# Kernel tuning notes

Hardware: AMD Instinct MI355X
Metric: run time of the kernel (lower is better)

The kernel has to match this reference:

```python
import jax, jax.numpy as jnp
import numpy as np

D_MODEL = 1024
N_HEADS = 16
D_K = D_MODEL // N_HEADS
THETA = 10000.0
B, S = 2, 2048


def _rope(x):
    # x: [B, H, S, Dh], interleaved-pair RoPE with positions arange(S)
    Dh = x.shape[-1]
    inv_freq = 1.0 / (THETA ** (jnp.arange(0, Dh, 2, dtype=jnp.float32) / Dh))  # [Dh/2]
    pos = jnp.arange(x.shape[-2], dtype=jnp.float32)
    ang = pos[:, None] * inv_freq[None, :]                      # [S, Dh/2]
    cos = jnp.repeat(jnp.cos(ang), 2, axis=-1).astype(x.dtype)  # [S, Dh]
    sin = jnp.repeat(jnp.sin(ang), 2, axis=-1).astype(x.dtype)
    # rotate pairs: (x_2k, x_2k+1) -> (-x_2k+1, x_2k)
    xp = x.reshape(*x.shape[:-1], Dh // 2, 2)
    rot = jnp.stack((-xp[..., 1], xp[..., 0]), axis=-1).reshape(x.shape)
    return x * cos + rot * sin


def setup_inputs() -> dict:
    key = jax.random.key(0)
    ks = jax.random.split(key, 5)
    std = (2.0 / (D_MODEL + D_MODEL)) ** 0.5
    return {
        "x": jax.random.normal(ks[0], (B, S, D_MODEL), dtype=jnp.float32),
        "wq": jax.random.normal(ks[1], (D_MODEL, D_MODEL), dtype=jnp.float32) * std,
        "wk": jax.random.normal(ks[2], (D_MODEL, D_MODEL), dtype=jnp.float32) * std,
        "wv": jax.random.normal(ks[3], (D_MODEL, D_MODEL), dtype=jnp.float32) * std,
        "wo": jax.random.normal(ks[4], (D_MODEL, D_MODEL), dtype=jnp.float32) * std,
    }


def reference(x, wq, wk, wv, wo):
    b, s, _ = x.shape
    def split_heads(t):
        return t.reshape(b, s, N_HEADS, D_K).transpose(0, 2, 1, 3)  # [B,H,S,Dk]
    # Linear: y = x @ W.T  (weights stored [out, in])
    q = split_heads(jnp.einsum('bsd,od->bso', x, wq))
    k = split_heads(jnp.einsum('bsd,od->bso', x, wk))
    v = split_heads(jnp.einsum('bsd,od->bso', x, wv))
    q = _rope(q)
    k = _rope(k)
    scores = jnp.einsum('bhqd,bhkd->bhqk', q, k) / jnp.sqrt(jnp.asarray(D_K, x.dtype))
    causal = jnp.tril(jnp.ones((s, s), dtype=bool))
    scores = jnp.where(causal[None, None], scores, -jnp.inf)
    attn = jax.nn.softmax(scores, axis=-1)
    out = jnp.einsum('bhqk,bhkd->bhqd', attn, v)
    out = out.transpose(0, 2, 1, 3).reshape(b, s, D_MODEL)
    return jnp.einsum('bsd,od->bso', out, wo)
```

## Files before the change

kernel.cpp:

```cpp
#include <hip/hip_runtime.h>


typedef unsigned short u16;
typedef __attribute__((ext_vector_type(8))) short short8;
typedef __attribute__((ext_vector_type(4))) float float4v;

typedef const __attribute__((address_space(1))) void GV;
typedef __attribute__((address_space(3))) void LV;

#define VSTR 72
#define QSCL 0.18033688011112042f

__device__ __forceinline__ u16 f2b(float f) {
    union { float f; unsigned int i; } t; t.f = f;
    unsigned int r = t.i + 0x7fffu + ((t.i >> 16) & 1u);
    return (u16)(r >> 16);
}

__global__ __launch_bounds__(256) void cvt_all(
    const float4* __restrict__ x,  const float4* __restrict__ wq,
    const float4* __restrict__ wk, const float4* __restrict__ wv,
    const float4* __restrict__ wo,
    u16* __restrict__ xb, u16* __restrict__ wcat, u16* __restrict__ wob)
{
    const int i = blockIdx.x * 256 + threadIdx.x;
    const float4* s; u16* d; int off;
    if (i < 524288) { s = x; d = xb; off = i; }
    else {
        const int widx = i - 524288;
        const int w = widx >> 17, o = widx & 131071;
        switch (w) {
            case 0:  s = wq; d = wcat;              break;
            case 1:  s = wk; d = wcat + (1 << 20);  break;
            case 2:  s = wv; d = wcat + (2 << 20);  break;
            default: s = wo; d = wob;               break;
        }
        off = o;
    }
    float4 a = s[2 * off], b = s[2 * off + 1];
    u16 t[8] = {f2b(a.x), f2b(a.y), f2b(a.z), f2b(a.w),
                f2b(b.x), f2b(b.y), f2b(b.z), f2b(b.w)};
    reinterpret_cast<int4*>(d)[off] = *reinterpret_cast<int4*>(t);
}

__global__ __launch_bounds__(256) void rope_tab(float2* __restrict__ tab) {
    const int i = blockIdx.x * 256 + threadIdx.x;
    const int pos = i >> 5, fi = i & 31;
    const float freq = exp2f((float)fi * -0.4152410118609203f);
    float sn, cs; sincosf((float)pos * freq, &sn, &cs);
    tab[i] = make_float2(cs, sn);
}

template<int NT, int ROPE, int NBLK>
__global__ __launch_bounds__(256) void gemm_tile(
    const u16* __restrict__ X, const u16* __restrict__ Wb,
    u16* __restrict__ Yq, u16* __restrict__ Yk, u16* __restrict__ Yv,
    float* __restrict__ Yf, const float2* __restrict__ tab)
{
    __shared__ u16 As[128 * 64];
    __shared__ u16 Bs[NT * 32 * 64];

    const int tid  = threadIdx.x;
    const int wave = tid >> 6;
    const int lane = tid & 63;
    const int quad = lane >> 4;
    const int l16  = lane & 15;
    const int wm = (wave >> 1) * 64, wn = (wave & 1) * (NT * 16);
    const int g = blockIdx.x;
    const int rr = g >> 3;
    const int m0 = ((g & 7) * 4 + rr / NBLK) * 128;
    const int n0 = (rr % NBLK) * (NT * 32);
    const int lrow = lane >> 3;
    const int cg8  = (lane & 7) ^ lrow;

    float4v acc[4][NT];
#pragma unroll
    for (int mt = 0; mt < 4; mt++)
#pragma unroll
        for (int nt = 0; nt < NT; nt++) acc[mt][nt] = (float4v){0.f, 0.f, 0.f, 0.f};

    for (int kb = 0; kb < 1024; kb += 64) {
        __syncthreads();
#pragma unroll
        for (int t = 0; t < 4; t++) {
            const int I = wave * 4 + t;
            const u16* gp = X + (size_t)(m0 + I * 8 + lrow) * 1024 + kb + cg8 * 8;
            __builtin_amdgcn_global_load_lds((GV*)gp, (LV*)&As[I * 512], 16, 0, 0);
        }
#pragma unroll
        for (int t = 0; t < NT; t++) {
            const int I = wave * NT + t;
            const u16* gp = Wb + (size_t)(n0 + I * 8 + lrow) * 1024 + kb + cg8 * 8;
            __builtin_amdgcn_global_load_lds((GV*)gp, (LV*)&Bs[I * 512], 16, 0, 0);
        }
        __syncthreads();
#pragma unroll
        for (int ks = 0; ks < 2; ks++) {
            const int su = ((ks * 4 + quad) ^ (l16 & 7)) * 8;
            short8 af[4], bf[NT];
#pragma unroll
            for (int t = 0; t < 4; t++)
                af[t] = *reinterpret_cast<const short8*>(&As[(wm + t * 16 + l16) * 64 + su]);
#pragma unroll
            for (int t = 0; t < NT; t++)
                bf[t] = *reinterpret_cast<const short8*>(&Bs[(wn + t * 16 + l16) * 64 + su]);
#pragma unroll
            for (int mt = 0; mt < 4; mt++)
#pragma unroll
                for (int nt = 0; nt < NT; nt++)
                    acc[mt][nt] = __builtin_amdgcn_mfma_f32_16x16x32_bf16(af[mt], bf[nt], acc[mt][nt], 0, 0, 0);
        }
    }

    if (ROPE) {
#pragma unroll
        for (int nt = 0; nt < NT; nt++) {
            const int cg = n0 + wn + nt * 16 + l16;
            const int buf = cg >> 10;
            const int c = cg & 1023;
            u16* dst = (buf == 0) ? Yq : ((buf == 1) ? Yk : Yv);
            const bool rp = (buf < 2);
            const float scl = (buf == 0) ? QSCL : 1.0f;
            const int fi = (cg & 63) >> 1;
#pragma unroll
            for (int mt = 0; mt < 4; mt++)
#pragma unroll
                for (int r = 0; r < 4; r++) {
                    const int row = m0 + wm + mt * 16 + quad * 4 + r;
                    float v = acc[mt][nt][r];
                    if (rp) {
                        const float2 t = tab[((row & 2047) << 5) + fi];
                        const float partner = __shfl_xor(v, 1);
                        v = (l16 & 1) ? fmaf(v, t.x,  partner * t.y)
                                      : fmaf(v, t.x, -partner * t.y);
                    }
                    dst[(size_t)row * 1024 + c] = f2b(v * scl);
                }
        }
    } else {
#pragma unroll
        for (int nt = 0; nt < NT; nt++) {
            const int col = n0 + wn + nt * 16 + l16;
#pragma unroll
            for (int mt = 0; mt < 4; mt++)
#pragma unroll
                for (int r = 0; r < 4; r++) {
                    const int row = m0 + wm + mt * 16 + quad * 4 + r;
                    Yf[(size_t)row * 1024 + col] = acc[mt][nt][r];
                }
        }
    }
}

__global__ __launch_bounds__(256, 2) void attn_kernel(
    const u16* Q, const u16* __restrict__ K,
    const u16* __restrict__ V, u16* O)
{
    __shared__ u16 Vt[64 * VSTR];
    __shared__ u16 Ps[4 * 16 * VSTR];

    const int tid  = threadIdx.x;
    const int wave = tid >> 6;
    const int lane = tid & 63;
    const int quad = lane >> 4;
    const int l16  = lane & 15;
    const int g = blockIdx.x;
    const int xcd = g & 7, slot = g >> 3;
    const int G = (slot >> 4) * 8 + xcd;
    const int qtA = slot & 15;
    const int qtB = 31 - qtA;
    const int b = G & 1, h = G >> 1;
    const size_t base = ((size_t)b * 2048) * 1024 + (size_t)h * 64;

    short8 qfA[2], qfB[2];
    {
        const size_t ra = base + (size_t)(qtA * 64 + wave * 16 + l16) * 1024;
        qfA[0] = *reinterpret_cast<const short8*>(Q + ra + quad * 8);
        qfA[1] = *reinterpret_cast<const short8*>(Q + ra + 32 + quad * 8);
        const size_t rb = base + (size_t)(qtB * 64 + wave * 16 + l16) * 1024;
        qfB[0] = *reinterpret_cast<const short8*>(Q + rb + quad * 8);
        qfB[1] = *reinterpret_cast<const short8*>(Q + rb + 32 + quad * 8);
    }

    float4v oA[4], oB[4];
#pragma unroll
    for (int i = 0; i < 4; i++) { oA[i] = (float4v){0.f,0.f,0.f,0.f}; oB[i] = (float4v){0.f,0.f,0.f,0.f}; }
    float sA[4] = {0.f,0.f,0.f,0.f}, sB[4] = {0.f,0.f,0.f,0.f};

    u16* Pw = Ps + wave * 16 * VSTR;
    const int srow = tid >> 2;
    const int cb   = (tid & 3) << 4;
    const int sxw  = srow ^ cb;

    const u16* Vp = V + base + (size_t)srow * 1024 + cb;
    const u16* kbase = K + base + (size_t)l16 * 1024 + quad * 8;
    int4 vr0 = *reinterpret_cast<const int4*>(Vp);
    int4 vr1 = *reinterpret_cast<const int4*>(Vp + 8);
    short8 kn[4][2], kc[4][2], vf[4][2];
#pragma unroll
    for (int nt = 0; nt < 4; nt++)
#pragma unroll
        for (int ks = 0; ks < 2; ks++)
            kn[nt][ks] = *reinterpret_cast<const short8*>(kbase + (size_t)(nt * 16) * 1024 + ks * 32);

    auto proc = [&](const short8 (&qf)[2], float4v (&oc)[4], float (&sr)[4], bool diag) {
        float4v sacc[4];
#pragma unroll
        for (int nt = 0; nt < 4; nt++) {
            sacc[nt] = (float4v){0.f, 0.f, 0.f, 0.f};
#pragma unroll
            for (int ks = 0; ks < 2; ks++)
                sacc[nt] = __builtin_amdgcn_mfma_f32_16x16x32_bf16(qf[ks], kc[nt][ks], sacc[nt], 0, 0, 0);
        }
#pragma unroll
        for (int r = 0; r < 4; r++) {
            const int qloc = wave * 16 + quad * 4 + r;
#pragma unroll
            for (int nt = 0; nt < 4; nt++) {
                float s = sacc[nt][r];
                if (diag && (nt * 16 + l16 > qloc)) s = -1e30f;
                const float p = exp2f(s);
                sr[r] += p;
                Pw[(quad * 4 + r) * VSTR + nt * 16 + l16] = f2b(p);
            }
        }
        __builtin_amdgcn_wave_barrier();
#pragma unroll
        for (int ks = 0; ks < 2; ks++) {
            short8 pf = *reinterpret_cast<const short8*>(&Pw[l16 * VSTR + ks * 32 + quad * 8]);
#pragma unroll
            for (int dt = 0; dt < 4; dt++)
                oc[dt] = __builtin_amdgcn_mfma_f32_16x16x32_bf16(pf, vf[dt][ks], oc[dt], 0, 0, 0);
        }
        __builtin_amdgcn_wave_barrier();
    };

    for (int j = 0; j <= qtB; j++) {
        __syncthreads();
        {
            const u16* a = reinterpret_cast<const u16*>(&vr0);
            const u16* c = reinterpret_cast<const u16*>(&vr1);
#pragma unroll
            for (int e = 0; e < 8; e++) Vt[(cb + e) * VSTR + sxw] = a[e];
#pragma unroll
            for (int e = 0; e < 8; e++) Vt[(cb + 8 + e) * VSTR + sxw] = c[e];
        }
#pragma unroll
        for (int nt = 0; nt < 4; nt++)
#pragma unroll
            for (int ks = 0; ks < 2; ks++) kc[nt][ks] = kn[nt][ks];
        __syncthreads();
        if (j < qtB) {
            Vp += 65536;
            vr0 = *reinterpret_cast<const int4*>(Vp);
            vr1 = *reinterpret_cast<const int4*>(Vp + 8);
            const u16* kb2 = kbase + (size_t)(j + 1) * 65536;
#pragma unroll
            for (int nt = 0; nt < 4; nt++)
#pragma unroll
                for (int ks = 0; ks < 2; ks++)
                    kn[nt][ks] = *reinterpret_cast<const short8*>(kb2 + (size_t)(nt * 16) * 1024 + ks * 32);
        }
#pragma unroll
        for (int nt = 0; nt < 4; nt++)
#pragma unroll
            for (int ks = 0; ks < 2; ks++)
                vf[nt][ks] = *reinterpret_cast<const short8*>(&Vt[(nt * 16 + l16) * VSTR + ((ks * 32 + quad * 8) ^ (nt << 4))]);
        if (j <= qtA) proc(qfA, oA, sA, j == qtA);
        proc(qfB, oB, sB, j == qtB);
    }

#pragma unroll
    for (int r = 0; r < 4; r++) {
        float la = sA[r], lb = sB[r];
#pragma unroll
        for (int msk = 1; msk < 16; msk <<= 1) { la += __shfl_xor(la, msk); lb += __shfl_xor(lb, msk); }
        const float invA = 1.0f / la, invB = 1.0f / lb;
        const int rloc = wave * 16 + quad * 4 + r;
        const size_t rowA = base + (size_t)(qtA * 64 + rloc) * 1024;
        const size_t rowB = base + (size_t)(qtB * 64 + rloc) * 1024;
#pragma unroll
        for (int dt = 0; dt < 4; dt++) {
            O[rowA + dt * 16 + l16] = f2b(oA[dt][r] * invA);
            O[rowB + dt * 16 + l16] = f2b(oB[dt][r] * invB);
        }
    }
}

extern "C" void kernel_launch(void* const* d_in, const int* in_sizes, int n_in,
                              void* d_out, int out_size, void* d_ws, size_t ws_size,
                              hipStream_t stream) {
    (void)in_sizes; (void)n_in; (void)out_size; (void)ws_size;
    const float* x  = (const float*)d_in[0];
    const float* wq = (const float*)d_in[1];
    const float* wk = (const float*)d_in[2];
    const float* wv = (const float*)d_in[3];
    const float* wo = (const float*)d_in[4];

    const size_t MN = (size_t)4096 * 1024;

    u16* xb   = (u16*)d_out;
    u16* wcat = xb + MN;
    float2* tab = (float2*)(wcat + (size_t)3072 * 1024);
    u16* qbuf = (u16*)d_ws;
    u16* kbuf = qbuf + MN;
    u16* vbuf = kbuf + MN;
    u16* wob  = vbuf + MN;

    cvt_all<<<4096, 256, 0, stream>>>((const float4*)x, (const float4*)wq,
                                      (const float4*)wk, (const float4*)wv,
                                      (const float4*)wo, xb, wcat, wob);
    rope_tab<<<256, 256, 0, stream>>>(tab);
    gemm_tile<4, 1, 24><<<768, 256, 0, stream>>>(xb, wcat, qbuf, kbuf, vbuf, nullptr, tab);
    attn_kernel<<<512, 256, 0, stream>>>(qbuf, kbuf, vbuf, qbuf);
    gemm_tile<2, 0, 16><<<512, 256, 0, stream>>>(qbuf, wob, nullptr, nullptr, nullptr, (float*)d_out, nullptr);
}
```

Before: 232.4 us.

## Split paired attention q-tiles into one tile per block with more occupancy

The attention kernel used to give each block two complementary causal query tiles (qtA and 31-qtA) that shared K/V loads. Now each block handles a single query tile, the grid is twice as large, and launch bounds allow four blocks per SIMD group instead of two. Block ordering alternates between descending and ascending tile indices across groups to spread the load. The goal is higher occupancy and fewer registers per thread. In exchange, the K/V reuse between the two paired tiles is lost, so global and LDS traffic for K/V roughly doubles, and per-block work becomes uneven.

New measurement: 289.3 us. +24.5%, slower.

```diff
diff --git a/kernel.cpp b/kernel.cpp
--- a/kernel.cpp
+++ b/kernel.cpp
@@ -152,7 +152,7 @@
     }
 }
 
-__global__ __launch_bounds__(256, 2) void attn_kernel(
+__global__ __launch_bounds__(256, 4) void attn_kernel(
     const u16* Q, const u16* __restrict__ K,
     const u16* __restrict__ V, u16* O)
 {
@@ -166,26 +166,24 @@
     const int l16  = lane & 15;
     const int g = blockIdx.x;
     const int xcd = g & 7, slot = g >> 3;
-    const int G = (slot >> 4) * 8 + xcd;
-    const int qtA = slot & 15;
-    const int qtB = 31 - qtA;
+    const int grp = slot >> 5;
+    const int i5  = slot & 31;
+    const int G = grp * 8 + xcd;
+    const int qt = (grp & 1) ? i5 : 31 - i5;
     const int b = G & 1, h = G >> 1;
     const size_t base = ((size_t)b * 2048) * 1024 + (size_t)h * 64;
 
-    short8 qfA[2], qfB[2];
+    short8 qf[2];
     {
-        const size_t ra = base + (size_t)(qtA * 64 + wave * 16 + l16) * 1024;
-        qfA[0] = *reinterpret_cast<const short8*>(Q + ra + quad * 8);
-        qfA[1] = *reinterpret_cast<const short8*>(Q + ra + 32 + quad * 8);
-        const size_t rb = base + (size_t)(qtB * 64 + wave * 16 + l16) * 1024;
-        qfB[0] = *reinterpret_cast<const short8*>(Q + rb + quad * 8);
-        qfB[1] = *reinterpret_cast<const short8*>(Q + rb + 32 + quad * 8);
-    }
-
-    float4v oA[4], oB[4];
-#pragma unroll
-    for (int i = 0; i < 4; i++) { oA[i] = (float4v){0.f,0.f,0.f,0.f}; oB[i] = (float4v){0.f,0.f,0.f,0.f}; }
-    float sA[4] = {0.f,0.f,0.f,0.f}, sB[4] = {0.f,0.f,0.f,0.f};
+        const size_t ra = base + (size_t)(qt * 64 + wave * 16 + l16) * 1024;
+        qf[0] = *reinterpret_cast<const short8*>(Q + ra + quad * 8);
+        qf[1] = *reinterpret_cast<const short8*>(Q + ra + 32 + quad * 8);
+    }
+
+    float4v o[4];
+#pragma unroll
+    for (int i = 0; i < 4; i++) o[i] = (float4v){0.f,0.f,0.f,0.f};
+    float s[4] = {0.f,0.f,0.f,0.f};
 
     u16* Pw = Ps + wave * 16 * VSTR;
     const int srow = tid >> 2;
@@ -203,7 +201,7 @@
         for (int ks = 0; ks < 2; ks++)
             kn[nt][ks] = *reinterpret_cast<const short8*>(kbase + (size_t)(nt * 16) * 1024 + ks * 32);
 
-    auto proc = [&](const short8 (&qf)[2], float4v (&oc)[4], float (&sr)[4], bool diag) {
+    auto proc = [&](bool diag) {
         float4v sacc[4];
 #pragma unroll
         for (int nt = 0; nt < 4; nt++) {
@@ -217,10 +215,10 @@
             const int qloc = wave * 16 + quad * 4 + r;
 #pragma unroll
             for (int nt = 0; nt < 4; nt++) {
-                float s = sacc[nt][r];
-                if (diag && (nt * 16 + l16 > qloc)) s = -1e30f;
-                const float p = exp2f(s);
-                sr[r] += p;
+                float sv = sacc[nt][r];
+                if (diag && (nt * 16 + l16 > qloc)) sv = -1e30f;
+                const float p = exp2f(sv);
+                s[r] += p;
                 Pw[(quad * 4 + r) * VSTR + nt * 16 + l16] = f2b(p);
             }
         }
@@ -230,12 +228,12 @@
             short8 pf = *reinterpret_cast<const short8*>(&Pw[l16 * VSTR + ks * 32 + quad * 8]);
 #pragma unroll
             for (int dt = 0; dt < 4; dt++)
-                oc[dt] = __builtin_amdgcn_mfma_f32_16x16x32_bf16(pf, vf[dt][ks], oc[dt], 0, 0, 0);
+                o[dt] = __builtin_amdgcn_mfma_f32_16x16x32_bf16(pf, vf[dt][ks], o[dt], 0, 0, 0);
         }
         __builtin_amdgcn_wave_barrier();
     };
 
-    for (int j = 0; j <= qtB; j++) {
+    for (int j = 0; j <= qt; j++) {
         __syncthreads();
         {
             const u16* a = reinterpret_cast<const u16*>(&vr0);
@@ -250,7 +248,7 @@
 #pragma unroll
             for (int ks = 0; ks < 2; ks++) kc[nt][ks] = kn[nt][ks];
         __syncthreads();
-        if (j < qtB) {
+        if (j < qt) {
             Vp += 65536;
             vr0 = *reinterpret_cast<const int4*>(Vp);
             vr1 = *reinterpret_cast<const int4*>(Vp + 8);
@@ -266,24 +264,20 @@
 #pragma unroll
             for (int ks = 0; ks < 2; ks++)
                 vf[nt][ks] = *reinterpret_cast<const short8*>(&Vt[(nt * 16 + l16) * VSTR + ((ks * 32 + quad * 8) ^ (nt << 4))]);
-        if (j <= qtA) proc(qfA, oA, sA, j == qtA);
-        proc(qfB, oB, sB, j == qtB);
+        proc(j == qt);
     }
 
 #pragma unroll
     for (int r = 0; r < 4; r++) {
-        float la = sA[r], lb = sB[r];
-#pragma unroll
-        for (int msk = 1; msk < 16; msk <<= 1) { la += __shfl_xor(la, msk); lb += __shfl_xor(lb, msk); }
-        const float invA = 1.0f / la, invB = 1.0f / lb;
+        float la = s[r];
+#pragma unroll
+        for (int msk = 1; msk < 16; msk <<= 1) la += __shfl_xor(la, msk);
+        const float inv = 1.0f / la;
         const int rloc = wave * 16 + quad * 4 + r;
-        const size_t rowA = base + (size_t)(qtA * 64 + rloc) * 1024;
-        const size_t rowB = base + (size_t)(qtB * 64 + rloc) * 1024;
-#pragma unroll
-        for (int dt = 0; dt < 4; dt++) {
-            O[rowA + dt * 16 + l16] = f2b(oA[dt][r] * invA);
-            O[rowB + dt * 16 + l16] = f2b(oB[dt][r] * invB);
-        }
+        const size_t row = base + (size_t)(qt * 64 + rloc) * 1024;
+#pragma unroll
+        for (int dt = 0; dt < 4; dt++)
+            O[row + dt * 16 + l16] = f2b(o[dt][r] * inv);
     }
 }
 
@@ -312,6 +306,6 @@
                                       (const float4*)wo, xb, wcat, wob);
     rope_tab<<<256, 256, 0, stream>>>(tab);
     gemm_tile<4, 1, 24><<<768, 256, 0, stream>>>(xb, wcat, qbuf, kbuf, vbuf, nullptr, tab);
-    attn_kernel<<<512, 256, 0, stream>>>(qbuf, kbuf, vbuf, qbuf);
+    attn_kernel<<<1024, 256, 0, stream>>>(qbuf, kbuf, vbuf, qbuf);
     gemm_tile<2, 0, 16><<<512, 256, 0, stream>>>(qbuf, wob, nullptr, nullptr, nullptr, (float*)d_out, nullptr);
 }
```
